# Performance work log

Hardware: AMD Instinct MI355X
Metric: run time of the kernel (lower is better)

## Reference

```python
import jax, jax.numpy as jnp
import numpy as np

N = 100_000   # nodes
E = 1_600_000 # edges
V = 100_000   # vocab
G = 256       # graphs in batch
D = 64        # emb/hidden dim


def setup_inputs() -> dict:
    key = jax.random.key(0)
    ks = jax.random.split(key, 12)
    x_tokens = jax.random.randint(ks[0], (N, 1), 0, V)
    edge_index = jax.random.randint(ks[1], (2, E), 0, N)
    batch = jnp.sort(jax.random.randint(ks[2], (N,), 0, G))
    s = 0.02
    return {
        "x_tokens": x_tokens,
        "edge_index": edge_index,
        "batch": batch,
        "emb_table": jax.random.normal(ks[3], (V, D), jnp.float32) * s,
        "W0": jax.random.normal(ks[4], (D, D), jnp.float32) * s,
        "b0": jnp.zeros((D,), jnp.float32),
        "W1": jax.random.normal(ks[5], (D, D), jnp.float32) * s,
        "b1": jnp.zeros((D,), jnp.float32),
        "W2": jax.random.normal(ks[6], (D, D), jnp.float32) * s,
        "b2": jnp.zeros((D,), jnp.float32),
        "Wc1": jax.random.normal(ks[7], (2 * D, D), jnp.float32) * s,
        "bc1": jnp.zeros((D,), jnp.float32),
        "Wc2": jax.random.normal(ks[8], (D, 2), jnp.float32) * s,
        "bc2": jnp.zeros((2,), jnp.float32),
    }


def _gcn_norm(edge_index, n_nodes):
    # add self loops, compute symmetric normalization coefficients
    loop = jnp.arange(n_nodes, dtype=edge_index.dtype)
    src = jnp.concatenate([edge_index[0], loop])
    dst = jnp.concatenate([edge_index[1], loop])
    deg = jax.ops.segment_sum(jnp.ones_like(dst, jnp.float32), dst, num_segments=n_nodes)
    dinv = jnp.where(deg > 0, deg ** -0.5, 0.0)
    norm = dinv[src] * dinv[dst]  # [E+N]
    return src, dst, norm


def _gcn_conv(x, W, b, src, dst, norm, n_nodes):
    x = x @ W                                   # [N, D]
    msg = x[src] * norm[:, None]                # gather + scale, [E+N, D]
    out = jax.ops.segment_sum(msg, dst, num_segments=n_nodes)
    return out + b


def reference(x_tokens, edge_index, batch, emb_table, W0, b0, W1, b1, W2, b2, Wc1, bc1, Wc2, bc2):
    n = x_tokens.shape[0]
    src, dst, norm = _gcn_norm(edge_index, n)
    x = emb_table[x_tokens[:, 0]]               # [N, D]
    for W, b in ((W0, b0), (W1, b1), (W2, b2)):
        x = jax.nn.relu(_gcn_conv(x, W, b, src, dst, norm, n))
    # dual pooling over graph ids
    cnt = jax.ops.segment_sum(jnp.ones((n,), x.dtype), batch, num_segments=G)
    h_sum = jax.ops.segment_sum(x, batch, num_segments=G)
    h_mean = h_sum / jnp.maximum(cnt, 1.0)[:, None]
    h_max = jax.ops.segment_max(x, batch, num_segments=G)
    h_max = jnp.where(jnp.isfinite(h_max), h_max, 0.0)
    h = jnp.concatenate([h_mean, h_max], axis=-1)   # [G, 2D]
    logits = jax.nn.relu(h @ Wc1 + bc1) @ Wc2 + bc2  # [G, 2]
    return logits
```

## Files before the change

### kernel.cpp

```cpp
#include <hip/hip_runtime.h>
#include <hip/hip_fp16.h>
#include <math.h>


#define BKT_LOG 9
#define BKT (1 << BKT_LOG)
#define CHUNK 4096

typedef _Float16 h2 __attribute__((ext_vector_type(2)));
typedef _Float16 f16x4 __attribute__((ext_vector_type(4)));
typedef _Float16 f16x8 __attribute__((ext_vector_type(8)));
typedef float f32x2 __attribute__((ext_vector_type(2)));
typedef float f32x4 __attribute__((ext_vector_type(4)));

union HU { unsigned u; h2 h; };
__device__ inline h2 h2bits(unsigned u) { HU x; x.u = u; return x.h; }

#if __has_builtin(__builtin_amdgcn_fdot2)
#define FDOT2(a, b, c) __builtin_amdgcn_fdot2((a), (b), (c), false)
#else
__device__ inline float FDOT2(h2 a, h2 b, float c) {
  return (float)a.x * (float)b.x + (float)a.y * (float)b.y + c;
}
#endif

#define MASK_X 0x00003C00u
#define MASK_Y 0x3C000000u

__device__ inline void acc4c(uint2 v, float& a0, float& a1, float& a2, float& a3) {
  h2 lo = h2bits(v.x), hi = h2bits(v.y);
  a0 = FDOT2(lo, h2bits(MASK_X), a0);
  a1 = FDOT2(lo, h2bits(MASK_Y), a1);
  a2 = FDOT2(hi, h2bits(MASK_X), a2);
  a3 = FDOT2(hi, h2bits(MASK_Y), a3);
}

#if __has_builtin(__builtin_amdgcn_cvt_pk_f32_fp8) && __has_builtin(__builtin_amdgcn_cvt_pk_fp8_f32)
#define HW_FP8 1
#else
#define HW_FP8 0
#endif

__device__ inline float fp8dec_sw(unsigned b) {
  unsigned s = (b >> 7) & 1, e = (b >> 3) & 15, m = b & 7;
  float v;
  if (e == 0) v = (float)m * 0.001953125f;
  else v = __uint_as_float(((e + 120u) << 23) | (m << 20));
  return s ? -v : v;
}
__device__ inline unsigned fp8enc_sw(float f) {
  unsigned s = (__float_as_uint(f) >> 31) << 7;
  float a = fabsf(f);
  if (!(a < 448.f)) return s | 0x7E;
  if (a < 0.0009765625f) return s;
  int e; float m = frexpf(a, &e);
  int E = e + 6;
  unsigned q;
  if (E <= 0) {
    q = (unsigned)lrintf(a * 512.f);
    if (q >= 8) return s | 0x08;
    return s | q;
  }
  q = (unsigned)lrintf((m * 2.f - 1.f) * 8.f);
  if (q == 8) { q = 0; E++; if (E > 15) return s | 0x7E; }
  return s | ((unsigned)E << 3) | q;
}

__device__ inline void acc4fp8(unsigned v, float& a0, float& a1, float& a2, float& a3) {
#if HW_FP8
  f32x2 lo = __builtin_amdgcn_cvt_pk_f32_fp8((int)v, false);
  f32x2 hi = __builtin_amdgcn_cvt_pk_f32_fp8((int)v, true);
  a0 += lo[0]; a1 += lo[1]; a2 += hi[0]; a3 += hi[1];
#else
  a0 += fp8dec_sw(v & 255u);
  a1 += fp8dec_sw((v >> 8) & 255u);
  a2 += fp8dec_sw((v >> 16) & 255u);
  a3 += fp8dec_sw((v >> 24) & 255u);
#endif
}

__device__ inline unsigned pk4fp8(float f0, float f1, float f2, float f3) {
#if HW_FP8
  int t = __builtin_amdgcn_cvt_pk_fp8_f32(f0, f1, 0, false);
  return (unsigned)__builtin_amdgcn_cvt_pk_fp8_f32(f2, f3, t, true);
#else
  return fp8enc_sw(f0) | (fp8enc_sw(f1) << 8) | (fp8enc_sw(f2) << 16) | (fp8enc_sw(f3) << 24);
#endif
}

__global__ __launch_bounds__(256) void k_wcvt(const float* __restrict__ W0,
                                              const float* __restrict__ W1,
                                              const float* __restrict__ W2,
                                              _Float16* __restrict__ Wf,
                                              int* __restrict__ gcur,
                                              float* __restrict__ hz, int hzn) {
  if (blockIdx.x < 3) {
    const float* W = (blockIdx.x == 0) ? W0 : (blockIdx.x == 1) ? W1 : W2;
    _Float16* out = Wf + blockIdx.x * 4096;
    for (int i = threadIdx.x; i < 4096; i += 256) {
      int c = i >> 10, s = (i >> 9) & 1, l = (i >> 3) & 63, j = i & 7;
      int k = 32 * s + 8 * (l >> 4) + j;
      int ncol = 16 * c + (l & 15);
      out[i] = (_Float16)W[k * 64 + ncol];
    }
  } else if (blockIdx.x == 3) {
    gcur[threadIdx.x] = 0;
  } else {
    for (int i = threadIdx.x; i < hzn; i += 256) hz[i] = 0.f;
  }
}

__global__ __launch_bounds__(256) void k_part(const int* __restrict__ src,
                                              const int* __restrict__ dst,
                                              int* __restrict__ gcur,
                                              int* __restrict__ ebuf,
                                              int E, int S) {
  __shared__ int pk[CHUNK];
  __shared__ unsigned short bk[CHUNK];
  __shared__ unsigned short sp[CHUNK];
  __shared__ int h[256], sc[256], base[256], cur[256];
  int tid = threadIdx.x;
  long c0 = (long)blockIdx.x * CHUNK;
  int m = (int)min((long)CHUNK, (long)E - c0);
  h[tid] = 0;
  __syncthreads();
  for (int i = tid; i < m; i += 256) {
    int s = src[c0 + i];
    int d = dst[c0 + i];
    int b = d >> BKT_LOG;
    pk[i] = ((d & (BKT - 1)) << 17) | s;
    bk[i] = (unsigned short)b;
    atomicAdd(&h[b], 1);
  }
  __syncthreads();
  int hv = h[tid];
  if (hv) base[tid] = atomicAdd(&gcur[tid], hv);
  sc[tid] = hv;
  __syncthreads();
  for (int d = 1; d < 256; d <<= 1) {
    int t = (tid >= d) ? sc[tid - d] : 0;
    __syncthreads();
    sc[tid] += t;
    __syncthreads();
  }
  cur[tid] = sc[tid] - hv;
  __syncthreads();
  for (int i = tid; i < m; i += 256) {
    int p = atomicAdd(&cur[bk[i]], 1);
    sp[p] = (unsigned short)i;
  }
  __syncthreads();
  for (int j = tid; j < m; j += 256) {
    int lo = 0, hi = 255;
    while (lo < hi) { int mid = (lo + hi) >> 1; if (sc[mid] > j) hi = mid; else lo = mid + 1; }
    int b = lo;
    int rel = j - (sc[b] - h[b]);
    int gpos = base[b] + rel;
    if (gpos < S)
      ebuf[(size_t)b * S + gpos] = pk[sp[j]];
  }
}

__global__ __launch_bounds__(512) void k_bplace(const int* __restrict__ ebuf,
                                                const int* __restrict__ gcur,
                                                int* __restrict__ off,
                                                int* __restrict__ eend,
                                                int* __restrict__ csrc,
                                                float* __restrict__ dinv,
                                                int N, int S) {
  __shared__ int s[512];
  __shared__ int cur[512];
  int b = blockIdx.x, tid = threadIdx.x;
  int n0 = b << BKT_LOG;
  int nn = min(BKT, N - n0);
  int e0 = b * S;
  int cnt = min(gcur[b], S - nn);
  s[tid] = (tid < nn) ? 1 : 0;
  __syncthreads();
  for (int e = tid; e < cnt; e += 512) atomicAdd(&s[ebuf[e0 + e] >> 17], 1);
  __syncthreads();
  int degws = s[tid];
  for (int d = 1; d < 512; d <<= 1) {
    int t = (tid >= d) ? s[tid - d] : 0;
    __syncthreads();
    s[tid] += t;
    __syncthreads();
  }
  int excl = s[tid] - degws;
  if (tid < nn) {
    off[n0 + tid] = e0 + excl;
    eend[n0 + tid] = e0 + excl + degws;
    dinv[n0 + tid] = 1.0f / sqrtf((float)degws);
    csrc[e0 + excl] = n0 + tid;
  }
  cur[tid] = excl + ((tid < nn) ? 1 : 0);
  __syncthreads();
  for (int e = tid; e < cnt; e += 512) {
    int p = ebuf[e0 + e];
    int pos = e0 + atomicAdd(&cur[p >> 17], 1);
    csrc[pos] = p & 0x1FFFF;
  }
}

template <bool EMB, bool F8>
__global__ __launch_bounds__(256) void k_mfmamm(const _Float16* __restrict__ y,
                                                const int* __restrict__ tok,
                                                const float* __restrict__ emb,
                                                const _Float16* __restrict__ Wf,
                                                const float* __restrict__ dinv,
                                                float scale,
                                                unsigned char* __restrict__ xh,
                                                int n) {
  __shared__ _Float16 lds[4 * 16 * 72];
  int w = threadIdx.x >> 6, l = threadIdx.x & 63;
  int m = l & 15, q = l >> 4;
  int rbase = blockIdx.x * 64 + w * 16;

  f16x8 a0, a1;
  if (EMB) {
    int node = min(rbase + m, n - 1);
    const float* er = emb + (size_t)tok[node] * 64;
    float4 v0 = *(const float4*)(er + q * 8);
    float4 v1 = *(const float4*)(er + q * 8 + 4);
    float4 v2 = *(const float4*)(er + 32 + q * 8);
    float4 v3 = *(const float4*)(er + 32 + q * 8 + 4);
    a0[0] = (_Float16)v0.x; a0[1] = (_Float16)v0.y; a0[2] = (_Float16)v0.z; a0[3] = (_Float16)v0.w;
    a0[4] = (_Float16)v1.x; a0[5] = (_Float16)v1.y; a0[6] = (_Float16)v1.z; a0[7] = (_Float16)v1.w;
    a1[0] = (_Float16)v2.x; a1[1] = (_Float16)v2.y; a1[2] = (_Float16)v2.z; a1[3] = (_Float16)v2.w;
    a1[4] = (_Float16)v3.x; a1[5] = (_Float16)v3.y; a1[6] = (_Float16)v3.z; a1[7] = (_Float16)v3.w;
  } else {
    int node = rbase + m;
    const _Float16* yr = y + ((size_t)(unsigned)node << 6);
    a0 = *(const f16x8*)(yr + q * 8);
    a1 = *(const f16x8*)(yr + 32 + q * 8);
  }
  float4 d4 = *(const float4*)(dinv + rbase + q * 4);

  const f16x8* wf = (const f16x8*)Wf + l;
  f32x4 acc[4];
#pragma unroll
  for (int c = 0; c < 4; c++) {
    f32x4 z = {0.f, 0.f, 0.f, 0.f};
    z = __builtin_amdgcn_mfma_f32_16x16x32_f16(a0, wf[(c * 2 + 0) * 64], z, 0, 0, 0);
    z = __builtin_amdgcn_mfma_f32_16x16x32_f16(a1, wf[(c * 2 + 1) * 64], z, 0, 0, 0);
    acc[c] = z;
  }

  const float ds[4] = {d4.x * scale, d4.y * scale, d4.z * scale, d4.w * scale};
  _Float16* ldw = lds + w * 16 * 72;
#pragma unroll
  for (int c = 0; c < 4; c++)
#pragma unroll
    for (int r = 0; r < 4; r++)
      ldw[(q * 4 + r) * 72 + c * 16 + m] = (_Float16)(acc[c][r] * ds[r]);
  __syncthreads();

  int row2 = l & 15, c2 = l >> 4;
  int node = rbase + row2;
  if (node < n) {
    if (F8) {
      const _Float16* sp16 = ldw + row2 * 72 + c2 * 16;
      unsigned wds[4];
#pragma unroll
      for (int k = 0; k < 4; k++)
        wds[k] = pk4fp8((float)sp16[4 * k + 0], (float)sp16[4 * k + 1],
                        (float)sp16[4 * k + 2], (float)sp16[4 * k + 3]);
      uint4 ov; ov.x = wds[0]; ov.y = wds[1]; ov.z = wds[2]; ov.w = wds[3];
      *(uint4*)(xh + ((size_t)(unsigned)node << 6) + c2 * 16) = ov;
    } else {
      const uint4* s4 = (const uint4*)(ldw + row2 * 72 + c2 * 16);
      uint4 v0 = s4[0], v1 = s4[1];
      uint4* dst = (uint4*)(xh + ((size_t)(unsigned)node << 7) + c2 * 32);
      dst[0] = v0;
      dst[1] = v1;
    }
  }
}

template <bool F8>
__global__ __launch_bounds__(256) void k_aggregate(const int* __restrict__ off,
                                                   const int* __restrict__ eend,
                                                   const int* __restrict__ csrc,
                                                   const float* __restrict__ dinv,
                                                   const unsigned char* __restrict__ xh,
                                                   const float* __restrict__ bias,
                                                   float invs,
                                                   _Float16* __restrict__ outp,
                                                   int n) {
  int lane = threadIdx.x & 63;
  int t = __builtin_amdgcn_readfirstlane(blockIdx.x * 4 + (threadIdx.x >> 6));
  if (t >= n) return;
  int e0 = off[t];
  int e1 = eend[t];
  int p = lane >> 4;
  int f = lane & 15;

  float a0 = 0.f, a1 = 0.f, a2 = 0.f, a3 = 0.f;
  for (int base = (e0 & ~7); base < e1; base += 32) {
    int my = base + p * 8;
    int4 iA = {0, 0, 0, 0}, iB = {0, 0, 0, 0};
    if (my < e1) iA = *(const int4*)(csrc + my);
    if (my + 4 < e1) iB = *(const int4*)(csrc + my + 4);
    if (F8) {
      unsigned v0 = 0, v1 = 0, v2 = 0, v3 = 0, v4 = 0, v5 = 0, v6 = 0, v7 = 0;
      if (my + 0 >= e0 && my + 0 < e1) v0 = *(const unsigned*)(xh + ((size_t)(unsigned)iA.x << 6) + f * 4);
      if (my + 1 >= e0 && my + 1 < e1) v1 = *(const unsigned*)(xh + ((size_t)(unsigned)iA.y << 6) + f * 4);
      if (my + 2 >= e0 && my + 2 < e1) v2 = *(const unsigned*)(xh + ((size_t)(unsigned)iA.z << 6) + f * 4);
      if (my + 3 >= e0 && my + 3 < e1) v3 = *(const unsigned*)(xh + ((size_t)(unsigned)iA.w << 6) + f * 4);
      if (my + 4 >= e0 && my + 4 < e1) v4 = *(const unsigned*)(xh + ((size_t)(unsigned)iB.x << 6) + f * 4);
      if (my + 5 >= e0 && my + 5 < e1) v5 = *(const unsigned*)(xh + ((size_t)(unsigned)iB.y << 6) + f * 4);
      if (my + 6 >= e0 && my + 6 < e1) v6 = *(const unsigned*)(xh + ((size_t)(unsigned)iB.z << 6) + f * 4);
      if (my + 7 >= e0 && my + 7 < e1) v7 = *(const unsigned*)(xh + ((size_t)(unsigned)iB.w << 6) + f * 4);
      acc4fp8(v0, a0, a1, a2, a3);
      acc4fp8(v1, a0, a1, a2, a3);
      acc4fp8(v2, a0, a1, a2, a3);
      acc4fp8(v3, a0, a1, a2, a3);
      acc4fp8(v4, a0, a1, a2, a3);
      acc4fp8(v5, a0, a1, a2, a3);
      acc4fp8(v6, a0, a1, a2, a3);
      acc4fp8(v7, a0, a1, a2, a3);
    } else {
      uint2 v0 = {0,0}, v1 = {0,0}, v2 = {0,0}, v3 = {0,0};
      uint2 v4 = {0,0}, v5 = {0,0}, v6 = {0,0}, v7 = {0,0};
      if (my + 0 >= e0 && my + 0 < e1) v0 = *(const uint2*)(xh + ((size_t)(unsigned)iA.x << 7) + f * 8);
      if (my + 1 >= e0 && my + 1 < e1) v1 = *(const uint2*)(xh + ((size_t)(unsigned)iA.y << 7) + f * 8);
      if (my + 2 >= e0 && my + 2 < e1) v2 = *(const uint2*)(xh + ((size_t)(unsigned)iA.z << 7) + f * 8);
      if (my + 3 >= e0 && my + 3 < e1) v3 = *(const uint2*)(xh + ((size_t)(unsigned)iA.w << 7) + f * 8);
      if (my + 4 >= e0 && my + 4 < e1) v4 = *(const uint2*)(xh + ((size_t)(unsigned)iB.x << 7) + f * 8);
      if (my + 5 >= e0 && my + 5 < e1) v5 = *(const uint2*)(xh + ((size_t)(unsigned)iB.y << 7) + f * 8);
      if (my + 6 >= e0 && my + 6 < e1) v6 = *(const uint2*)(xh + ((size_t)(unsigned)iB.z << 7) + f * 8);
      if (my + 7 >= e0 && my + 7 < e1) v7 = *(const uint2*)(xh + ((size_t)(unsigned)iB.w << 7) + f * 8);
      acc4c(v0, a0, a1, a2, a3);
      acc4c(v1, a0, a1, a2, a3);
      acc4c(v2, a0, a1, a2, a3);
      acc4c(v3, a0, a1, a2, a3);
      acc4c(v4, a0, a1, a2, a3);
      acc4c(v5, a0, a1, a2, a3);
      acc4c(v6, a0, a1, a2, a3);
      acc4c(v7, a0, a1, a2, a3);
    }
  }

  a0 += __shfl_xor(a0, 16); a0 += __shfl_xor(a0, 32);
  a1 += __shfl_xor(a1, 16); a1 += __shfl_xor(a1, 32);
  a2 += __shfl_xor(a2, 16); a2 += __shfl_xor(a2, 32);
  a3 += __shfl_xor(a3, 16); a3 += __shfl_xor(a3, 32);

  if (p == 0) {
    float sc = dinv[t] * invs;
    float4 bb = *(const float4*)(bias + f * 4);
    f16x4 hv;
    hv[0] = (_Float16)(fmaxf(a0 * sc + bb.x, 0.f) * 4096.f);
    hv[1] = (_Float16)(fmaxf(a1 * sc + bb.y, 0.f) * 4096.f);
    hv[2] = (_Float16)(fmaxf(a2 * sc + bb.z, 0.f) * 4096.f);
    hv[3] = (_Float16)(fmaxf(a3 * sc + bb.w, 0.f) * 4096.f);
    *(f16x4*)((char*)outp + ((size_t)(unsigned)t << 7) + f * 8) = hv;
  }
}

__global__ __launch_bounds__(256) void k_pool(const _Float16* __restrict__ x,
                                              const int* __restrict__ batch,
                                              float* __restrict__ hsum,
                                              float* __restrict__ hmax,
                                              int* __restrict__ cntg,
                                              int n) {
  int wid = (blockIdx.x * blockDim.x + threadIdx.x) >> 6;
  int lane = threadIdx.x & 63;
  int i0 = wid * 64;
  if (i0 >= n) return;
  int i1 = min(i0 + 64, n);
  int batch_l = (i0 + lane < n) ? batch[i0 + lane] : 0;
  float gsum = 0.f, gmax = 0.f;
  int cur = __shfl(batch_l, 0);
  int c = 0;
  for (int i = i0; i < i1; i++) {
    int g = __shfl(batch_l, i - i0);
    if (g != cur) {
      atomicAdd(&hsum[cur * 64 + lane], gsum);
      atomicMax((int*)&hmax[cur * 64 + lane], __float_as_int(gmax));
      if (lane == 0) atomicAdd(&cntg[cur], c);
      gsum = 0.f; gmax = 0.f; c = 0; cur = g;
    }
    float v = (float)x[((size_t)(unsigned)i << 6) + lane];
    gsum += v;
    gmax = fmaxf(gmax, v);
    c++;
  }
  atomicAdd(&hsum[cur * 64 + lane], gsum);
  atomicMax((int*)&hmax[cur * 64 + lane], __float_as_int(gmax));
  if (lane == 0) atomicAdd(&cntg[cur], c);
}

__global__ __launch_bounds__(64) void k_cls(const float* __restrict__ hsum,
                                            const float* __restrict__ hmax,
                                            const int* __restrict__ cnt,
                                            const float* __restrict__ Wc1,
                                            const float* __restrict__ bc1,
                                            const float* __restrict__ Wc2,
                                            const float* __restrict__ bc2,
                                            float* __restrict__ out) {
  __shared__ float h[128];
  __shared__ float hid[64];
  int g = blockIdx.x, j = threadIdx.x;
  int c = cnt[g];
  float cf = (float)(c > 0 ? c : 1);
  h[j] = hsum[g * 64 + j] / cf * (1.0f / 4096.0f);
  h[64 + j] = hmax[g * 64 + j] * (1.0f / 4096.0f);
  __syncthreads();
  float acc = bc1[j];
  for (int k = 0; k < 128; k++) acc += h[k] * Wc1[k * 64 + j];
  hid[j] = fmaxf(acc, 0.f);
  __syncthreads();
  if (j < 2) {
    float a = bc2[j];
    for (int k = 0; k < 64; k++) a += hid[k] * Wc2[k * 2 + j];
    out[g * 2 + j] = a;
  }
}

extern "C" void kernel_launch(void* const* d_in, const int* in_sizes, int n_in,
                              void* d_out, int out_size, void* d_ws, size_t ws_size,
                              hipStream_t stream) {
  const int N = in_sizes[0];
  const int E = in_sizes[1] / 2;
  const int G = out_size / 2;
  const int B = (N + BKT - 1) >> BKT_LOG;
  const int Npad = (N + 63) & ~63;
  const int S = ((((E + B - 1) / B) * 3 / 2 + 256) + 7) & ~7;

  const int* tok   = (const int*)d_in[0];
  const int* ei    = (const int*)d_in[1];
  const int* batch = (const int*)d_in[2];
  const float* emb = (const float*)d_in[3];
  const float* W0 = (const float*)d_in[4];  const float* b0 = (const float*)d_in[5];
  const float* W1 = (const float*)d_in[6];  const float* b1 = (const float*)d_in[7];
  const float* W2 = (const float*)d_in[8];  const float* b2 = (const float*)d_in[9];
  const float* Wc1 = (const float*)d_in[10]; const float* bc1 = (const float*)d_in[11];
  const float* Wc2 = (const float*)d_in[12]; const float* bc2 = (const float*)d_in[13];
  const int* srcp = ei;
  const int* dstp = ei + E;

  int* off    = (int*)d_ws;
  int* eend   = off + N;
  float* dinv = (float*)(eend + N);
  int* gcur   = (int*)(dinv + Npad);
  _Float16* Wf = (_Float16*)(gcur + 256);
  int* csrc   = (int*)(Wf + 3 * 4096);
  unsigned char* xh = (unsigned char*)(csrc + (size_t)B * S);
  _Float16* y  = (_Float16*)(xh + (size_t)Npad * 128);
  int* ebuf   = (int*)y;
  float* hsum = (float*)(y + (size_t)Npad * 64);
  float* hmax = hsum + (size_t)G * 64;
  int*   cntg = (int*)(hmax + (size_t)G * 64);

  auto cdiv = [](long a, long b) { return (int)((a + b - 1) / b); };
  const int aggBlocks = cdiv(N, 4);

  k_wcvt<<<5, 256, 0, stream>>>(W0, W1, W2, Wf, gcur, hsum, G * 129);

  k_part<<<cdiv(E, CHUNK), 256, 0, stream>>>(srcp, dstp, gcur, ebuf, E, S);
  k_bplace<<<B, 512, 0, stream>>>(ebuf, gcur, off, eend, csrc, dinv, N, S);

  k_mfmamm<true, true><<<cdiv(N, 64), 256, 0, stream>>>(nullptr, tok, emb, Wf, dinv, 256.f, xh, N);
  k_aggregate<true><<<aggBlocks, 256, 0, stream>>>(off, eend, csrc, dinv, xh, b0, 1.f / 256.f, y, N);

  k_mfmamm<false, true><<<cdiv(N, 64), 256, 0, stream>>>(y, nullptr, nullptr, Wf + 4096, dinv, 1.0f, xh, N);
  k_aggregate<true><<<aggBlocks, 256, 0, stream>>>(off, eend, csrc, dinv, xh, b1, 1.f / 4096.f, y, N);

  k_mfmamm<false, false><<<cdiv(N, 64), 256, 0, stream>>>(y, nullptr, nullptr, Wf + 8192, dinv, 1.f / 16.f, xh, N);
  k_aggregate<false><<<aggBlocks, 256, 0, stream>>>(off, eend, csrc, dinv, xh, b2, 1.f / 256.f, y, N);

  k_pool<<<cdiv(N, 256), 256, 0, stream>>>(y, batch, hsum, hmax, cntg, N);

  k_cls<<<G, 64, 0, stream>>>(hsum, hmax, cntg, Wc1, bc1, Wc2, bc2, (float*)d_out);
}
```

Measured before the change: 321.4 us.

## Make aggregate kernel persistent with software-prefetched next-node edge indices

The aggregation kernel becomes grid-strided with a fixed grid of 2048 blocks, so each wavefront processes several destination nodes in turn. While it works on the current node, it prefetches the CSR offsets two nodes ahead and the first eight column indices of the next node, aiming to hide the dependent off->csrc->xh load latency. In exchange it uses more registers and runs fewer waves than the previous one-node-per-wave launch, which may reduce latency hiding through occupancy.

```diff
diff --git a/kernel.cpp b/kernel.cpp
--- a/kernel.cpp
+++ b/kernel.cpp
@@ -86,6 +86,50 @@
 #else
   return fp8enc_sw(f0) | (fp8enc_sw(f1) << 8) | (fp8enc_sw(f2) << 16) | (fp8enc_sw(f3) << 24);
 #endif
+}
+
+template <bool F8>
+__device__ inline void rows8(const unsigned char* __restrict__ xh, int my,
+                             int e0, int e1, int f, int4 iA, int4 iB,
+                             float& a0, float& a1, float& a2, float& a3) {
+  if (F8) {
+    unsigned v0 = 0, v1 = 0, v2 = 0, v3 = 0, v4 = 0, v5 = 0, v6 = 0, v7 = 0;
+    if (my + 0 >= e0 && my + 0 < e1) v0 = *(const unsigned*)(xh + ((size_t)(unsigned)iA.x << 6) + f * 4);
+    if (my + 1 >= e0 && my + 1 < e1) v1 = *(const unsigned*)(xh + ((size_t)(unsigned)iA.y << 6) + f * 4);
+    if (my + 2 >= e0 && my + 2 < e1) v2 = *(const unsigned*)(xh + ((size_t)(unsigned)iA.z << 6) + f * 4);
+    if (my + 3 >= e0 && my + 3 < e1) v3 = *(const unsigned*)(xh + ((size_t)(unsigned)iA.w << 6) + f * 4);
+    if (my + 4 >= e0 && my + 4 < e1) v4 = *(const unsigned*)(xh + ((size_t)(unsigned)iB.x << 6) + f * 4);
+    if (my + 5 >= e0 && my + 5 < e1) v5 = *(const unsigned*)(xh + ((size_t)(unsigned)iB.y << 6) + f * 4);
+    if (my + 6 >= e0 && my + 6 < e1) v6 = *(const unsigned*)(xh + ((size_t)(unsigned)iB.z << 6) + f * 4);
+    if (my + 7 >= e0 && my + 7 < e1) v7 = *(const unsigned*)(xh + ((size_t)(unsigned)iB.w << 6) + f * 4);
+    acc4fp8(v0, a0, a1, a2, a3);
+    acc4fp8(v1, a0, a1, a2, a3);
+    acc4fp8(v2, a0, a1, a2, a3);
+    acc4fp8(v3, a0, a1, a2, a3);
+    acc4fp8(v4, a0, a1, a2, a3);
+    acc4fp8(v5, a0, a1, a2, a3);
+    acc4fp8(v6, a0, a1, a2, a3);
+    acc4fp8(v7, a0, a1, a2, a3);
+  } else {
+    uint2 v0 = {0,0}, v1 = {0,0}, v2 = {0,0}, v3 = {0,0};
+    uint2 v4 = {0,0}, v5 = {0,0}, v6 = {0,0}, v7 = {0,0};
+    if (my + 0 >= e0 && my + 0 < e1) v0 = *(const uint2*)(xh + ((size_t)(unsigned)iA.x << 7) + f * 8);
+    if (my + 1 >= e0 && my + 1 < e1) v1 = *(const uint2*)(xh + ((size_t)(unsigned)iA.y << 7) + f * 8);
+    if (my + 2 >= e0 && my + 2 < e1) v2 = *(const uint2*)(xh + ((size_t)(unsigned)iA.z << 7) + f * 8);
+    if (my + 3 >= e0 && my + 3 < e1) v3 = *(const uint2*)(xh + ((size_t)(unsigned)iA.w << 7) + f * 8);
+    if (my + 4 >= e0 && my + 4 < e1) v4 = *(const uint2*)(xh + ((size_t)(unsigned)iB.x << 7) + f * 8);
+    if (my + 5 >= e0 && my + 5 < e1) v5 = *(const uint2*)(xh + ((size_t)(unsigned)iB.y << 7) + f * 8);
+    if (my + 6 >= e0 && my + 6 < e1) v6 = *(const uint2*)(xh + ((size_t)(unsigned)iB.z << 7) + f * 8);
+    if (my + 7 >= e0 && my + 7 < e1) v7 = *(const uint2*)(xh + ((size_t)(unsigned)iB.w << 7) + f * 8);
+    acc4c(v0, a0, a1, a2, a3);
+    acc4c(v1, a0, a1, a2, a3);
+    acc4c(v2, a0, a1, a2, a3);
+    acc4c(v3, a0, a1, a2, a3);
+    acc4c(v4, a0, a1, a2, a3);
+    acc4c(v5, a0, a1, a2, a3);
+    acc4c(v6, a0, a1, a2, a3);
+    acc4c(v7, a0, a1, a2, a3);
+  }
 }
 
 __global__ __launch_bounds__(256) void k_wcvt(const float* __restrict__ W0,
@@ -286,75 +330,64 @@
                                                    const float* __restrict__ bias,
                                                    float invs,
                                                    _Float16* __restrict__ outp,
-                                                   int n) {
+                                                   int n, int stride) {
   int lane = threadIdx.x & 63;
+  int p = lane >> 4;
+  int f = lane & 15;
   int t = __builtin_amdgcn_readfirstlane(blockIdx.x * 4 + (threadIdx.x >> 6));
   if (t >= n) return;
-  int e0 = off[t];
-  int e1 = eend[t];
-  int p = lane >> 4;
-  int f = lane & 15;
-
-  float a0 = 0.f, a1 = 0.f, a2 = 0.f, a3 = 0.f;
-  for (int base = (e0 & ~7); base < e1; base += 32) {
-    int my = base + p * 8;
-    int4 iA = {0, 0, 0, 0}, iB = {0, 0, 0, 0};
+
+  int e0 = off[t], e1 = eend[t];
+  int4 iA = {0, 0, 0, 0}, iB = {0, 0, 0, 0};
+  {
+    int my = (e0 & ~7) + p * 8;
     if (my < e1) iA = *(const int4*)(csrc + my);
     if (my + 4 < e1) iB = *(const int4*)(csrc + my + 4);
-    if (F8) {
-      unsigned v0 = 0, v1 = 0, v2 = 0, v3 = 0, v4 = 0, v5 = 0, v6 = 0, v7 = 0;
-      if (my + 0 >= e0 && my + 0 < e1) v0 = *(const unsigned*)(xh + ((size_t)(unsigned)iA.x << 6) + f * 4);
-      if (my + 1 >= e0 && my + 1 < e1) v1 = *(const unsigned*)(xh + ((size_t)(unsigned)iA.y << 6) + f * 4);
-      if (my + 2 >= e0 && my + 2 < e1) v2 = *(const unsigned*)(xh + ((size_t)(unsigned)iA.z << 6) + f * 4);
-      if (my + 3 >= e0 && my + 3 < e1) v3 = *(const unsigned*)(xh + ((size_t)(unsigned)iA.w << 6) + f * 4);
-      if (my + 4 >= e0 && my + 4 < e1) v4 = *(const unsigned*)(xh + ((size_t)(unsigned)iB.x << 6) + f * 4);
-      if (my + 5 >= e0 && my + 5 < e1) v5 = *(const unsigned*)(xh + ((size_t)(unsigned)iB.y << 6) + f * 4);
-      if (my + 6 >= e0 && my + 6 < e1) v6 = *(const unsigned*)(xh + ((size_t)(unsigned)iB.z << 6) + f * 4);
-      if (my + 7 >= e0 && my + 7 < e1) v7 = *(const unsigned*)(xh + ((size_t)(unsigned)iB.w << 6) + f * 4);
-      acc4fp8(v0, a0, a1, a2, a3);
-      acc4fp8(v1, a0, a1, a2, a3);
-      acc4fp8(v2, a0, a1, a2, a3);
-      acc4fp8(v3, a0, a1, a2, a3);
-      acc4fp8(v4, a0, a1, a2, a3);
-      acc4fp8(v5, a0, a1, a2, a3);
-      acc4fp8(v6, a0, a1, a2, a3);
-      acc4fp8(v7, a0, a1, a2, a3);
-    } else {
-      uint2 v0 = {0,0}, v1 = {0,0}, v2 = {0,0}, v3 = {0,0};
-      uint2 v4 = {0,0}, v5 = {0,0}, v6 = {0,0}, v7 = {0,0};
-      if (my + 0 >= e0 && my + 0 < e1) v0 = *(const uint2*)(xh + ((size_t)(unsigned)iA.x << 7) + f * 8);
-      if (my + 1 >= e0 && my + 1 < e1) v1 = *(const uint2*)(xh + ((size_t)(unsigned)iA.y << 7) + f * 8);
-      if (my + 2 >= e0 && my + 2 < e1) v2 = *(const uint2*)(xh + ((size_t)(unsigned)iA.z << 7) + f * 8);
-      if (my + 3 >= e0 && my + 3 < e1) v3 = *(const uint2*)(xh + ((size_t)(unsigned)iA.w << 7) + f * 8);
-      if (my + 4 >= e0 && my + 4 < e1) v4 = *(const uint2*)(xh + ((size_t)(unsigned)iB.x << 7) + f * 8);
-      if (my + 5 >= e0 && my + 5 < e1) v5 = *(const uint2*)(xh + ((size_t)(unsigned)iB.y << 7) + f * 8);
-      if (my + 6 >= e0 && my + 6 < e1) v6 = *(const uint2*)(xh + ((size_t)(unsigned)iB.z << 7) + f * 8);
-      if (my + 7 >= e0 && my + 7 < e1) v7 = *(const uint2*)(xh + ((size_t)(unsigned)iB.w << 7) + f * 8);
-      acc4c(v0, a0, a1, a2, a3);
-      acc4c(v1, a0, a1, a2, a3);
-      acc4c(v2, a0, a1, a2, a3);
-      acc4c(v3, a0, a1, a2, a3);
-      acc4c(v4, a0, a1, a2, a3);
-      acc4c(v5, a0, a1, a2, a3);
-      acc4c(v6, a0, a1, a2, a3);
-      acc4c(v7, a0, a1, a2, a3);
+  }
+  int tn = t + stride;
+  int e0n = 0, e1n = 0;
+  if (tn < n) { e0n = off[tn]; e1n = eend[tn]; }
+
+  while (true) {
+    int4 iAn = {0, 0, 0, 0}, iBn = {0, 0, 0, 0};
+    if (tn < n) {
+      int myn = (e0n & ~7) + p * 8;
+      if (myn < e1n) iAn = *(const int4*)(csrc + myn);
+      if (myn + 4 < e1n) iBn = *(const int4*)(csrc + myn + 4);
     }
-  }
-
-  a0 += __shfl_xor(a0, 16); a0 += __shfl_xor(a0, 32);
-  a1 += __shfl_xor(a1, 16); a1 += __shfl_xor(a1, 32);
-  a2 += __shfl_xor(a2, 16); a2 += __shfl_xor(a2, 32);
-  a3 += __shfl_xor(a3, 16); a3 += __shfl_xor(a3, 32);
-
-  if (p == 0) {
-    float sc = dinv[t] * invs;
-    float4 bb = *(const float4*)(bias + f * 4);
-    f16x4 hv;
-    hv[0] = (_Float16)(fmaxf(a0 * sc + bb.x, 0.f) * 4096.f);
-    hv[1] = (_Float16)(fmaxf(a1 * sc + bb.y, 0.f) * 4096.f);
-    hv[2] = (_Float16)(fmaxf(a2 * sc + bb.z, 0.f) * 4096.f);
-    hv[3] = (_Float16)(fmaxf(a3 * sc + bb.w, 0.f) * 4096.f);
-    *(f16x4*)((char*)outp + ((size_t)(unsigned)t << 7) + f * 8) = hv;
+    int tnn = tn + stride;
+    int e0nn = 0, e1nn = 0;
+    if (tnn < n) { e0nn = off[tnn]; e1nn = eend[tnn]; }
+
+    float a0 = 0.f, a1 = 0.f, a2 = 0.f, a3 = 0.f;
+    int base0 = e0 & ~7;
+    rows8<F8>(xh, base0 + p * 8, e0, e1, f, iA, iB, a0, a1, a2, a3);
+    for (int base = base0 + 32; base < e1; base += 32) {
+      int my = base + p * 8;
+      int4 jA = {0, 0, 0, 0}, jB = {0, 0, 0, 0};
+      if (my < e1) jA = *(const int4*)(csrc + my);
+      if (my + 4 < e1) jB = *(const int4*)(csrc + my + 4);
+      rows8<F8>(xh, my, e0, e1, f, jA, jB, a0, a1, a2, a3);
+    }
+
+    a0 += __shfl_xor(a0, 16); a0 += __shfl_xor(a0, 32);
+    a1 += __shfl_xor(a1, 16); a1 += __shfl_xor(a1, 32);
+    a2 += __shfl_xor(a2, 16); a2 += __shfl_xor(a2, 32);
+    a3 += __shfl_xor(a3, 16); a3 += __shfl_xor(a3, 32);
+    if (p == 0) {
+      float sc = dinv[t] * invs;
+      float4 bb = *(const float4*)(bias + f * 4);
+      f16x4 hv;
+      hv[0] = (_Float16)(fmaxf(a0 * sc + bb.x, 0.f) * 4096.f);
+      hv[1] = (_Float16)(fmaxf(a1 * sc + bb.y, 0.f) * 4096.f);
+      hv[2] = (_Float16)(fmaxf(a2 * sc + bb.z, 0.f) * 4096.f);
+      hv[3] = (_Float16)(fmaxf(a3 * sc + bb.w, 0.f) * 4096.f);
+      *(f16x4*)((char*)outp + ((size_t)(unsigned)t << 7) + f * 8) = hv;
+    }
+
+    if (tn >= n) break;
+    t = tn; e0 = e0n; e1 = e1n; iA = iAn; iB = iBn;
+    tn = tnn; e0n = e0nn; e1n = e1nn;
   }
 }
 
@@ -454,7 +487,8 @@
   int*   cntg = (int*)(hmax + (size_t)G * 64);
 
   auto cdiv = [](long a, long b) { return (int)((a + b - 1) / b); };
-  const int aggBlocks = cdiv(N, 4);
+  const int aggBlocks = 2048;
+  const int aggStride = aggBlocks * 4;
 
   k_wcvt<<<5, 256, 0, stream>>>(W0, W1, W2, Wf, gcur, hsum, G * 129);
 
@@ -462,13 +496,13 @@
   k_bplace<<<B, 512, 0, stream>>>(ebuf, gcur, off, eend, csrc, dinv, N, S);
 
   k_mfmamm<true, true><<<cdiv(N, 64), 256, 0, stream>>>(nullptr, tok, emb, Wf, dinv, 256.f, xh, N);
-  k_aggregate<true><<<aggBlocks, 256, 0, stream>>>(off, eend, csrc, dinv, xh, b0, 1.f / 256.f, y, N);
+  k_aggregate<true><<<aggBlocks, 256, 0, stream>>>(off, eend, csrc, dinv, xh, b0, 1.f / 256.f, y, N, aggStride);
 
   k_mfmamm<false, true><<<cdiv(N, 64), 256, 0, stream>>>(y, nullptr, nullptr, Wf + 4096, dinv, 1.0f, xh, N);
-  k_aggregate<true><<<aggBlocks, 256, 0, stream>>>(off, eend, csrc, dinv, xh, b1, 1.f / 4096.f, y, N);
+  k_aggregate<true><<<aggBlocks, 256, 0, stream>>>(off, eend, csrc, dinv, xh, b1, 1.f / 4096.f, y, N, aggStride);
 
   k_mfmamm<false, false><<<cdiv(N, 64), 256, 0, stream>>>(y, nullptr, nullptr, Wf + 8192, dinv, 1.f / 16.f, xh, N);
-  k_aggregate<false><<<aggBlocks, 256, 0, stream>>>(off, eend, csrc, dinv, xh, b2, 1.f / 256.f, y, N);
+  k_aggregate<false><<<aggBlocks, 256, 0, stream>>>(off, eend, csrc, dinv, xh, b2, 1.f / 256.f, y, N, aggStride);
 
   k_pool<<<cdiv(N, 256), 256, 0, stream>>>(y, batch, hsum, hmax, cntg, N);
 
```

Result: faster. 304.6 us (median of 3 runs) (-5.2%).
